# Kernel optimization log

Measured on AMD Instinct MI355X. Metric: run time of the kernel, lower is better.

The kernel has to match this reference:

```python
import jax, jax.numpy as jnp
import numpy as np
import math
from jax import lax

HID, H, K = 1024, 8, 4
D = HID // H
B, T = 2, 2048
CLAMP_MAX = 0.999995
LN_EPS = 1e-5

def _logit(x):
    x = min(max(x, 1e-06), 1 - 1e-06)
    return math.log(x / (1 - x))

def setup_inputs() -> dict:
    key = jax.random.key(0)
    ks = jax.random.split(key, 8)
    def xavier(k, fan_in, fan_out):
        s = math.sqrt(2.0 / (fan_in + fan_out))
        return jax.random.normal(k, (fan_in, fan_out), jnp.float32) * s
    x = jax.random.normal(ks[0], (B, T, HID), jnp.float32)
    mask = jnp.ones((B, T), jnp.float32)
    Wq = xavier(ks[1], HID, HID)
    Wk = xavier(ks[2], HID, HID)
    Wv = xavier(ks[3], HID, HID)
    Wb = xavier(ks[4], HID, H)
    bb = jnp.full((H,), _logit(0.99), jnp.float32)
    Wm = xavier(ks[5], HID, H * K)
    bm = jnp.zeros((H * K,), jnp.float32)
    Wo = xavier(ks[6], HID, HID)
    bo = jnp.zeros((HID,), jnp.float32)
    base = np.array([_logit(math.exp(-1.0 / t)) for t in [16.0, 64.0, 256.0, 1024.0]], np.float32)
    base_logit = jnp.asarray(np.tile(base[None, :], (H, 1)))  # (H, K)
    ln_g = jnp.ones((HID,), jnp.float32)
    ln_b = jnp.zeros((HID,), jnp.float32)
    return dict(x=x, mask=mask, Wq=Wq, Wk=Wk, Wv=Wv, Wb=Wb, bb=bb, Wm=Wm, bm=bm,
                Wo=Wo, bo=bo, base_logit=base_logit, ln_g=ln_g, ln_b=ln_b)

def _delta_scan(q, k, v, beta, mix, mask, base_logit):
    # q,k,v: (B,T,H,D); beta: (B,T,H); mix: (B,T,H,K); mask: (B,T)
    b, t = q.shape[0], q.shape[1]
    base_r = jax.nn.sigmoid(base_logit)  # (H,K)
    state0 = jnp.zeros((b, H, K, D, D), jnp.float32)

    def step(state, inp):
        q_t, k_t, v_t, b_t, mix_t, m_t = inp
        valid = (m_t > 0)[:, None, None, None, None]            # (B,1,1,1,1)
        r_eff = jnp.clip(b_t[:, :, None] * base_r[None], 0.0, CLAMP_MAX)  # (B,H,K)
        outer = jnp.einsum('bhd,bhe->bhde', k_t, v_t)[:, :, None]          # (B,H,1,D,D)
        new_state = jnp.where(valid, state * r_eff[..., None, None] + outer, state)
        o_scales = jnp.einsum('bhd,bhkde->bhke', q_t, new_state)           # (B,H,K,D)
        w = jax.nn.softmax(mix_t, axis=-1)                                  # (B,H,K)
        o_t = jnp.sum(w[..., None] * o_scales, axis=2)                      # (B,H,D)
        o_t = o_t * (m_t > 0)[:, None, None].astype(o_t.dtype)
        return new_state, o_t

    xs = (jnp.moveaxis(q, 1, 0), jnp.moveaxis(k, 1, 0), jnp.moveaxis(v, 1, 0),
          jnp.moveaxis(beta, 1, 0), jnp.moveaxis(mix, 1, 0), jnp.moveaxis(mask, 1, 0))
    _, outs = lax.scan(step, state0, xs)       # (T,B,H,D)
    return jnp.moveaxis(outs, 0, 1)            # (B,T,H,D)

def reference(x, mask, Wq, Wk, Wv, Wb, bb, Wm, bm, Wo, bo, base_logit, ln_g, ln_b):
    b, t, _ = x.shape
    def elu1(z):
        return jax.nn.elu(z) + 1.0
    q = elu1((x @ Wq).reshape(b, t, H, D))
    k = elu1((x @ Wk).reshape(b, t, H, D))
    v = (x @ Wv).reshape(b, t, H, D)
    beta = jax.nn.sigmoid(x @ Wb + bb)               # (B,T,H)
    mix = (x @ Wm + bm).reshape(b, t, H, K)          # (B,T,H,K)
    head_out = _delta_scan(q, k, v, beta, mix, mask, base_logit)  # (B,T,H,D)
    out = head_out.reshape(b, t, HID) @ Wo + bo
    y = x + out                                       # residual (dropout in eval mode)
    mu = jnp.mean(y, axis=-1, keepdims=True)
    var = jnp.mean((y - mu) ** 2, axis=-1, keepdims=True)
    return (y - mu) * lax.rsqrt(var + LN_EPS) * ln_g + ln_b
```

## Files before the change

### kernel.cpp

```cpp
#include <hip/hip_runtime.h>
#include <hip/hip_bf16.h>
#include <math.h>

#define TSEQ 2048
#define NHID 1024

typedef float f32x4 __attribute__((ext_vector_type(4)));
typedef __bf16 bf16x8 __attribute__((ext_vector_type(8)));

static __device__ __forceinline__ unsigned short f2bf(float f) {
  unsigned u = __float_as_uint(f);
  u += 0x7fffu + ((u >> 16) & 1u);
  return (unsigned short)(u >> 16);
}
static __device__ __forceinline__ float bf2f(unsigned short h) {
  return __uint_as_float(((unsigned)h) << 16);
}

#define GLDS16(g, l) __builtin_amdgcn_global_load_lds( \
    (const __attribute__((address_space(1))) unsigned int*)(g), \
    (__attribute__((address_space(3))) unsigned int*)(l), 16, 0, 0)

__global__ __launch_bounds__(256) void transpose_all_kernel(
    const float* __restrict__ Wq, const float* __restrict__ Wk,
    const float* __restrict__ Wv, const float* __restrict__ Wo,
    unsigned short* __restrict__ Wqkvt, unsigned short* __restrict__ Wto) {
  __shared__ float tile[32][33];
  const float* W;
  unsigned short* Wt;
  int m = blockIdx.z;
  if (m == 0)      { W = Wq; Wt = Wqkvt; }
  else if (m == 1) { W = Wk; Wt = Wqkvt + 1024 * 1024; }
  else if (m == 2) { W = Wv; Wt = Wqkvt + 2 * 1024 * 1024; }
  else             { W = Wo; Wt = Wto; }
  int bx = blockIdx.x * 32;
  int by = blockIdx.y * 32;
  int tx = threadIdx.x, ty = threadIdx.y;
#pragma unroll
  for (int i = 0; i < 32; i += 8)
    tile[ty + i][tx] = W[(size_t)(by + ty + i) * NHID + bx + tx];
  __syncthreads();
#pragma unroll
  for (int i = 0; i < 32; i += 8)
    Wt[(size_t)(bx + ty + i) * NHID + by + tx] = f2bf(tile[tx][ty + i]);
}

template <int MODE>
__global__ __launch_bounds__(256) void gemm_pipe_kernel(
    const unsigned short* __restrict__ A, const unsigned short* __restrict__ Bt,
    unsigned short* __restrict__ Oq, unsigned short* __restrict__ Ok,
    unsigned short* __restrict__ Ov, float* __restrict__ P0, float* __restrict__ P1) {
  __shared__ __align__(16) unsigned short As[3 * 4096];
  __shared__ __align__(16) unsigned short Bs[3 * 4096];
  const int tid = threadIdx.x;
  const int lane = tid & 63;
  const int wave = tid >> 6;
  const int wr = wave >> 1, wc = wave & 1;
  const int rowBase = blockIdx.y * 128;
  const int colBase = blockIdx.x * 128;
  const int NT = (MODE == 0) ? 32 : 16;
  const int kOff = (MODE == 0) ? 0 : blockIdx.z * 512;

  const int c0 = wave * 128 + lane;
  const int c1 = c0 + 64;
  const int r0 = c0 >> 2, kc0 = (c0 & 3) ^ ((r0 >> 1) & 3);
  const int r1 = c1 >> 2, kc1 = (c1 & 3) ^ ((r1 >> 1) & 3);
  const unsigned short* gA0 = A + (size_t)(rowBase + r0) * 1024 + kOff + kc0 * 8;
  const unsigned short* gA1 = A + (size_t)(rowBase + r1) * 1024 + kOff + kc1 * 8;
  const unsigned short* gB0 = Bt + (size_t)(colBase + r0) * 1024 + kOff + kc0 * 8;
  const unsigned short* gB1 = Bt + (size_t)(colBase + r1) * 1024 + kOff + kc1 * 8;
  const int wofs = wave * 1024;

  const int kq = lane >> 4;
  const int r16 = lane & 15;

  f32x4 acc[4][4] = {};

#define STAGE(buf, k0)                                       \
  do {                                                       \
    GLDS16(gA0 + (k0), &As[(buf) * 4096 + wofs]);            \
    GLDS16(gA1 + (k0), &As[(buf) * 4096 + wofs + 512]);      \
    GLDS16(gB0 + (k0), &Bs[(buf) * 4096 + wofs]);            \
    GLDS16(gB1 + (k0), &Bs[(buf) * 4096 + wofs + 512]);      \
  } while (0)

  STAGE(0, 0);
  STAGE(1, 32);
  int cur = 0, stg = 2;
  for (int t = 0; t < NT; ++t) {
    if (t < NT - 2) {
      STAGE(stg, (t + 2) * 32);
      asm volatile("s_waitcnt vmcnt(8)" ::: "memory");
    } else if (t == NT - 2) {
      asm volatile("s_waitcnt vmcnt(4)" ::: "memory");
    } else {
      asm volatile("s_waitcnt vmcnt(0)" ::: "memory");
    }
    __builtin_amdgcn_s_barrier();
    asm volatile("" ::: "memory");
    const unsigned short* Ac = &As[cur * 4096];
    const unsigned short* Bc = &Bs[cur * 4096];
    bf16x8 af[4], bfr[4];
#pragma unroll
    for (int m = 0; m < 4; ++m) {
      int row = wr * 64 + m * 16 + r16;
      af[m] = *(const bf16x8*)(Ac + row * 32 + (kq ^ ((row >> 1) & 3)) * 8);
      int colr = wc * 64 + m * 16 + r16;
      bfr[m] = *(const bf16x8*)(Bc + colr * 32 + (kq ^ ((colr >> 1) & 3)) * 8);
    }
#pragma unroll
    for (int m = 0; m < 4; ++m)
#pragma unroll
      for (int n = 0; n < 4; ++n)
        acc[m][n] = __builtin_amdgcn_mfma_f32_16x16x32_bf16(af[m], bfr[n], acc[m][n], 0, 0, 0);
    asm volatile("" ::: "memory");
    __builtin_amdgcn_s_barrier();
    asm volatile("" ::: "memory");
    cur = (cur == 2) ? 0 : cur + 1;
    stg = (stg == 2) ? 0 : stg + 1;
  }
#undef STAGE

  const int r4 = (lane >> 4) * 4;
  if (MODE == 1) {
    float* P = (blockIdx.z == 0) ? P0 : P1;
#pragma unroll
    for (int m = 0; m < 4; ++m)
#pragma unroll
      for (int n = 0; n < 4; ++n) {
        int col = colBase + wc * 64 + n * 16 + r16;
#pragma unroll
        for (int j = 0; j < 4; ++j) {
          int row = rowBase + wr * 64 + m * 16 + r4 + j;
          P[(size_t)row * 1024 + col] = acc[m][n][j];
        }
      }
  } else {
    unsigned short* outp;
    int cb;
    bool elu;
    if (colBase < 1024)      { outp = Oq; cb = colBase;        elu = true;  }
    else if (colBase < 2048) { outp = Ok; cb = colBase - 1024; elu = true;  }
    else                     { outp = Ov; cb = colBase - 2048; elu = false; }
#pragma unroll
    for (int m = 0; m < 4; ++m)
#pragma unroll
      for (int n = 0; n < 4; ++n) {
        int col = cb + wc * 64 + n * 16 + r16;
#pragma unroll
        for (int j = 0; j < 4; ++j) {
          int row = rowBase + wr * 64 + m * 16 + r4 + j;
          float v = acc[m][n][j];
          if (elu) v = (v > 0.f) ? (v + 1.f) : expf(v);
          outp[(size_t)row * 1024 + col] = f2bf(v);
        }
      }
  }
}

__global__ __launch_bounds__(256) void pack_wbm_kernel(const float* __restrict__ Wb,
    const float* __restrict__ Wm, float* __restrict__ Wt) {
  int id = blockIdx.x * 256 + threadIdx.x;
  if (id >= 40960) return;
  int o = id >> 10, i = id & 1023;
  Wt[id] = (o < 8) ? Wb[i * 8 + o] : Wm[i * 32 + (o - 8)];
}

__global__ __launch_bounds__(256) void rw8_kernel(const float* __restrict__ x,
    const float* __restrict__ Wt, const float* __restrict__ bb,
    const float* __restrict__ bm, const float* __restrict__ base_logit,
    float* __restrict__ R, float* __restrict__ Wsm,
    unsigned short* __restrict__ Xb) {
  __shared__ float xs[8][1024];
  __shared__ float outs[8][40];
  int row0 = blockIdx.x * 8;
  int tid = threadIdx.x;
#pragma unroll
  for (int r = 0; r < 8; ++r) {
    float4 xv = *(const float4*)(x + (size_t)(row0 + r) * 1024 + tid * 4);
    *(float4*)(&xs[r][tid * 4]) = xv;
    ushort4 xo;
    xo.x = f2bf(xv.x); xo.y = f2bf(xv.y); xo.z = f2bf(xv.z); xo.w = f2bf(xv.w);
    *(ushort4*)(Xb + (size_t)(row0 + r) * 1024 + tid * 4) = xo;
  }
  __syncthreads();
  int wave = tid >> 6, lane = tid & 63;
  for (int o = wave; o < 40; o += 4) {
    const float* wr = Wt + o * 1024;
    float w[16];
#pragma unroll
    for (int it = 0; it < 16; ++it) w[it] = wr[it * 64 + lane];
#pragma unroll
    for (int r = 0; r < 8; ++r) {
      float sum = 0.f;
#pragma unroll
      for (int it = 0; it < 16; ++it) sum += xs[r][it * 64 + lane] * w[it];
#pragma unroll
      for (int off = 32; off > 0; off >>= 1) sum += __shfl_down(sum, off);
      if (lane == 0) outs[r][o] = sum;
    }
  }
  __syncthreads();
  {
    int r = tid >> 5, j = tid & 31;
    int row = row0 + r;
    int h = j >> 2;
    float beta = 1.f / (1.f + expf(-(outs[r][h] + bb[h])));
    float br = 1.f / (1.f + expf(-base_logit[j]));
    float rr = fminf(fmaxf(beta * br, 0.f), 0.999995f);
    float mval = outs[r][8 + j] + bm[j];
    float mx = fmaxf(mval, __shfl_xor(mval, 1));
    mx = fmaxf(mx, __shfl_xor(mx, 2));
    float ex = expf(mval - mx);
    float ssum = ex + __shfl_xor(ex, 1);
    ssum += __shfl_xor(ssum, 2);
    R[(size_t)row * 32 + j] = rr;
    Wsm[(size_t)row * 32 + j] = ex / ssum;
  }
}

__global__ __launch_bounds__(256) void decay2_kernel(const float* __restrict__ R,
    const float* __restrict__ Wsm, const float* __restrict__ mask,
    float* __restrict__ WA, float* __restrict__ IA, float* __restrict__ DU,
    float* __restrict__ AC) {
  int wave = threadIdx.x >> 6, lane = threadIdx.x & 63;
  int id = blockIdx.x * 4 + wave;
  int c = id & 15, k = (id >> 4) & 3, bh = id >> 6;
  int b = bh >> 3, h = bh & 7;
  int row0 = b * TSEQ + c * 128 + 2 * lane;
  float m0 = mask[row0], m1 = mask[row0 + 1];
  size_t i0 = (size_t)row0 * 32 + h * 4 + k;
  float rr0 = (m0 > 0.f) ? R[i0] : 1.f;
  float rr1 = (m1 > 0.f) ? R[i0 + 32] : 1.f;
  float incl = rr0 * rr1;
#pragma unroll
  for (int off = 1; off < 64; off <<= 1) {
    float o = __shfl_up(incl, off);
    if (lane >= off) incl *= o;
  }
  float excl = __shfl_up(incl, 1);
  if (lane == 0) excl = 1.f;
  float a0 = fmaxf(excl * rr0, 1e-25f);
  float a1 = fmaxf(a0 * rr1, 1e-25f);
  float aC = __shfl(a1, 63);
  if (lane == 63) AC[(bh * 16 + c) * 4 + k] = a1;
  bool v0 = m0 > 0.f, v1 = m1 > 0.f;
  float w0 = Wsm[i0], w1 = Wsm[i0 + 32];
  int dub = ((bh * 16 + c) * 4 + k) * 128 + 2 * lane;
  WA[i0] = v0 ? w0 * a0 : 0.f;
  WA[i0 + 32] = v1 ? w1 * a1 : 0.f;
  IA[i0] = v0 ? 1.f / a0 : 0.f;
  IA[i0 + 32] = v1 ? 1.f / a1 : 0.f;
  DU[dub] = v0 ? aC / a0 : 0.f;
  DU[dub + 1] = v1 ? aC / a1 : 0.f;
}

__global__ __launch_bounds__(512) void chunkA_kernel(
    const unsigned short* __restrict__ Qb, const unsigned short* __restrict__ Kb,
    const unsigned short* __restrict__ Vb,
    const float* __restrict__ WA, const float* __restrict__ IA,
    const float* __restrict__ DU,
    float* __restrict__ Olocal, unsigned short* __restrict__ UT) {
  __shared__ __align__(16) char KTl[32768];
  __shared__ __align__(16) char VTl[32768];
  __shared__ __align__(16) char Pl[32768];
  __shared__ __align__(16) float WAl[128][4];
  __shared__ __align__(16) float IAl[128][4];
  __shared__ float DUl[4][128];

  int wg = blockIdx.x;
  int bh = wg >> 4, c = wg & 15;
  int b = bh >> 3, h = bh & 7;
  int t0 = c * 128;
  int tid = threadIdx.x;
  int lane = tid & 63, wave = tid >> 6;
  int wbase = wave * 16;
  int l15 = lane & 15, lq = lane >> 4;

  const size_t qkvbase = ((size_t)b * TSEQ + t0) * 1024 + h * 128;

  for (int it = 0; it < 4; ++it) {
    int ci = tid + it * 512;
    int t = ci >> 4, s = ci & 15;
    bf16x8 kv = *(const bf16x8*)(Kb + qkvbase + (size_t)t * 1024 + s * 8);
    bf16x8 vv = *(const bf16x8*)(Vb + qkvbase + (size_t)t * 1024 + s * 8);
#pragma unroll
    for (int e = 0; e < 8; ++e) {
      int d = s * 8 + e;
      int off = d * 256 + (((t >> 3) ^ (d & 7)) << 4) + (t & 7) * 2;
      *(unsigned short*)(KTl + off) = f2bf((float)kv[e]);
      *(unsigned short*)(VTl + off) = f2bf((float)vv[e]);
    }
  }
  {
    int t = tid >> 2, k = tid & 3;
    size_t idx = ((size_t)b * TSEQ + t0 + t) * 32 + h * 4 + k;
    WAl[t][k] = WA[idx];
    IAl[t][k] = IA[idx];
    int k2 = tid >> 7, j = tid & 127;
    DUl[k2][j] = DU[((bh * 16 + c) * 4 + k2) * 128 + j];
  }
  __syncthreads();

  bf16x8 qf[4];
#pragma unroll
  for (int ds = 0; ds < 4; ++ds)
    qf[ds] = *(const bf16x8*)(Qb + qkvbase + (size_t)(wbase + l15) * 1024 + ds * 32 + lq * 8);
  f32x4 accP[8];
#pragma unroll
  for (int jf = 0; jf < 8; ++jf) {
    f32x4 a = {};
#pragma unroll
    for (int ds = 0; ds < 4; ++ds) {
      bf16x8 kfrag = *(const bf16x8*)(Kb + qkvbase + (size_t)(jf * 16 + l15) * 1024 + ds * 32 + lq * 8);
      a = __builtin_amdgcn_mfma_f32_16x16x32_bf16(qf[ds], kfrag, a, 0, 0, 0);
    }
    accP[jf] = a;
  }

  float4 wa4[4];
#pragma unroll
  for (int jj = 0; jj < 4; ++jj)
    wa4[jj] = *(const float4*)&WAl[wbase + lq * 4 + jj][0];
#pragma unroll
  for (int jf = 0; jf < 8; ++jf) {
    float4 ia4 = *(const float4*)&IAl[jf * 16 + l15][0];
#pragma unroll
    for (int jj = 0; jj < 4; ++jj) {
      int tl = wbase + lq * 4 + jj;
      int jl = jf * 16 + l15;
      float m = 0.f;
      if (jl <= tl)
        m = wa4[jj].x * ia4.x + wa4[jj].y * ia4.y + wa4[jj].z * ia4.z + wa4[jj].w * ia4.w;
      float pv = accP[jf][jj] * m;
      int off = tl * 256 + (((jl >> 3) ^ (tl & 7)) << 4) + (jl & 7) * 2;
      *(unsigned short*)(Pl + off) = f2bf(pv);
    }
  }

  bf16x8 pf[4];
#pragma unroll
  for (int js = 0; js < 4; ++js) {
    int tl = wbase + l15;
    int slot = js * 4 + lq;
    pf[js] = *(const bf16x8*)(Pl + tl * 256 + ((slot ^ (tl & 7)) << 4));
  }
#pragma unroll
  for (int dvf = 0; dvf < 8; ++dvf) {
    f32x4 a = {};
    int dv = dvf * 16 + l15;
#pragma unroll
    for (int js = 0; js < 4; ++js) {
      int slot = js * 4 + lq;
      bf16x8 vfrag = *(const bf16x8*)(VTl + dv * 256 + ((slot ^ (dv & 7)) << 4));
      a = __builtin_amdgcn_mfma_f32_16x16x32_bf16(pf[js], vfrag, a, 0, 0, 0);
    }
#pragma unroll
    for (int jj = 0; jj < 4; ++jj) {
      int tl = wbase + lq * 4 + jj;
      Olocal[((size_t)b * TSEQ + t0 + tl) * 1024 + h * 128 + dv] = a[jj];
    }
  }

  if (c < 15) {
#pragma unroll 1
    for (int k = 0; k < 4; ++k) {
      f32x4 accU[8] = {};
#pragma unroll 1
      for (int js = 0; js < 4; ++js) {
        int dvr = wbase + l15;
        int slot = js * 4 + lq;
        bf16x8 af = *(const bf16x8*)(VTl + dvr * 256 + ((slot ^ (dvr & 7)) << 4));
        int j0 = js * 32 + lq * 8;
        bf16x8 afs;
#pragma unroll
        for (int e = 0; e < 8; ++e)
          afs[e] = (__bf16)((float)af[e] * DUl[k][j0 + e]);
#pragma unroll
        for (int dkf = 0; dkf < 8; ++dkf) {
          int dk = dkf * 16 + l15;
          bf16x8 kf = *(const bf16x8*)(KTl + dk * 256 + ((slot ^ (dk & 7)) << 4));
          accU[dkf] = __builtin_amdgcn_mfma_f32_16x16x32_bf16(afs, kf, accU[dkf], 0, 0, 0);
        }
      }
      size_t ub = (((size_t)bh * 16 + c) * 4 + k) * 16384;
#pragma unroll
      for (int dkf = 0; dkf < 8; ++dkf) {
        int dk = dkf * 16 + l15;
#pragma unroll
        for (int jj = 0; jj < 4; ++jj) {
          int dvr = wbase + lq * 4 + jj;
          UT[ub + (size_t)dvr * 128 + dk] = f2bf(accU[dkf][jj]);
        }
      }
    }
  }
}

__global__ __launch_bounds__(256) void chainB_kernel(const unsigned short* __restrict__ UT,
    const float* __restrict__ AC, unsigned short* __restrict__ S0T) {
  int id = blockIdx.x * 256 + threadIdx.x;
  int dk = id & 127;
  int dv = (id >> 7) & 127;
  int k = (id >> 14) & 3;
  int bh = id >> 16;
  size_t elem = (size_t)dv * 128 + dk;
  float S = 0.f;
#pragma unroll 1
  for (int c = 0; c < 15; ++c) {
    size_t ub = (((size_t)bh * 16 + c) * 4 + k) * 16384;
    float u = bf2f(UT[ub + elem]);
    float aC = AC[(bh * 16 + c) * 4 + k];
    S = aC * S + u;
    size_t sb = (((size_t)bh * 16 + (c + 1)) * 4 + k) * 16384;
    S0T[sb + elem] = f2bf(S);
  }
}

__global__ __launch_bounds__(512) void chunkC_kernel(const unsigned short* __restrict__ Qb,
    const unsigned short* __restrict__ S0T, const float* __restrict__ WA,
    const float* __restrict__ Olocal, unsigned short* __restrict__ Ob) {
  __shared__ __align__(16) char Sl[32768];
  int wg = blockIdx.x;
  int bh = wg >> 4, c = wg & 15;
  int b = bh >> 3, h = bh & 7;
  int t0 = c * 128;
  int tid = threadIdx.x, lane = tid & 63, wave = tid >> 6;
  int l15 = lane & 15, lq = lane >> 4, wbase = wave * 16;
  size_t qbase = ((size_t)b * TSEQ + t0) * 1024 + h * 128;

  f32x4 accO[8] = {};
  if (c > 0) {
    int tl = wbase + l15;
#pragma unroll 1
    for (int k = 0; k < 4; ++k) {
      __syncthreads();
      size_t sb = (((size_t)bh * 16 + c) * 4 + k) * 16384;
      for (int it = 0; it < 4; ++it) {
        int ci = tid + it * 512;
        int dv = ci >> 4, s = ci & 15;
        bf16x8 vv = *(const bf16x8*)(S0T + sb + (size_t)dv * 128 + s * 8);
        *(bf16x8*)(Sl + dv * 256 + ((s ^ (dv & 7)) << 4)) = vv;
      }
      __syncthreads();
      float sc = WA[((size_t)b * TSEQ + t0 + tl) * 32 + h * 4 + k];
#pragma unroll 1
      for (int ds = 0; ds < 4; ++ds) {
        bf16x8 qf = *(const bf16x8*)(Qb + qbase + (size_t)tl * 1024 + ds * 32 + lq * 8);
        bf16x8 qs;
#pragma unroll
        for (int e = 0; e < 8; ++e) qs[e] = (__bf16)((float)qf[e] * sc);
#pragma unroll
        for (int dvf = 0; dvf < 8; ++dvf) {
          int dv = dvf * 16 + l15;
          int slot = ds * 4 + lq;
          bf16x8 sf = *(const bf16x8*)(Sl + dv * 256 + ((slot ^ (dv & 7)) << 4));
          accO[dvf] = __builtin_amdgcn_mfma_f32_16x16x32_bf16(qs, sf, accO[dvf], 0, 0, 0);
        }
      }
    }
  }
#pragma unroll
  for (int dvf = 0; dvf < 8; ++dvf) {
    int dv = dvf * 16 + l15;
#pragma unroll
    for (int jj = 0; jj < 4; ++jj) {
      int tl = wbase + lq * 4 + jj;
      size_t off = ((size_t)b * TSEQ + t0 + tl) * 1024 + h * 128 + dv;
      Ob[off] = f2bf(accO[dvf][jj] + Olocal[off]);
    }
  }
}

__global__ __launch_bounds__(256) void ln_kernel(const float* __restrict__ P0,
    const float* __restrict__ P1, const float* __restrict__ bo,
    const float* __restrict__ xres,
    const float* __restrict__ g, const float* __restrict__ bta,
    float* __restrict__ out) {
  int row = blockIdx.x;
  int tid = threadIdx.x;
  int lane = tid & 63, wave = tid >> 6;
  __shared__ float red[8];
  size_t base = (size_t)row * 1024 + tid * 4;
  float4 a = *(const float4*)(P0 + base);
  float4 b2 = *(const float4*)(P1 + base);
  float4 xv = *(const float4*)(xres + base);
  float4 bv = *(const float4*)(bo + tid * 4);
  float4 v;
  v.x = a.x + b2.x + bv.x + xv.x;
  v.y = a.y + b2.y + bv.y + xv.y;
  v.z = a.z + b2.z + bv.z + xv.z;
  v.w = a.w + b2.w + bv.w + xv.w;
  float sum = v.x + v.y + v.z + v.w;
#pragma unroll
  for (int off = 32; off > 0; off >>= 1) sum += __shfl_down(sum, off);
  if (lane == 0) red[wave] = sum;
  __syncthreads();
  float mu = (red[0] + red[1] + red[2] + red[3]) * (1.f / 1024.f);
  float4 d;
  d.x = v.x - mu; d.y = v.y - mu; d.z = v.z - mu; d.w = v.w - mu;
  float sq = d.x * d.x + d.y * d.y + d.z * d.z + d.w * d.w;
#pragma unroll
  for (int off = 32; off > 0; off >>= 1) sq += __shfl_down(sq, off);
  __syncthreads();
  if (lane == 0) red[4 + wave] = sq;
  __syncthreads();
  float var = (red[4] + red[5] + red[6] + red[7]) * (1.f / 1024.f);
  float inv = rsqrtf(var + 1e-5f);
  float4 gg = *(const float4*)(g + tid * 4);
  float4 bb4 = *(const float4*)(bta + tid * 4);
  float4 o;
  o.x = d.x * inv * gg.x + bb4.x;
  o.y = d.y * inv * gg.y + bb4.y;
  o.z = d.z * inv * gg.z + bb4.z;
  o.w = d.w * inv * gg.w + bb4.w;
  *(float4*)(out + (size_t)row * 1024 + tid * 4) = o;
}

extern "C" void kernel_launch(void* const* d_in, const int* in_sizes, int n_in,
                              void* d_out, int out_size, void* d_ws, size_t ws_size,
                              hipStream_t stream) {
  const float* x    = (const float*)d_in[0];
  const float* mask = (const float*)d_in[1];
  const float* Wq   = (const float*)d_in[2];
  const float* Wk   = (const float*)d_in[3];
  const float* Wv   = (const float*)d_in[4];
  const float* Wb   = (const float*)d_in[5];
  const float* bb   = (const float*)d_in[6];
  const float* Wm   = (const float*)d_in[7];
  const float* bm   = (const float*)d_in[8];
  const float* Wo   = (const float*)d_in[9];
  const float* bo   = (const float*)d_in[10];
  const float* base_logit = (const float*)d_in[11];
  const float* ln_g = (const float*)d_in[12];
  const float* ln_b = (const float*)d_in[13];

  char* ws = (char*)d_ws;
  const size_t MB = 1024u * 1024u;
  unsigned short* Xb    = (unsigned short*)(ws + 0);
  unsigned short* Wqkvt = (unsigned short*)(ws + 8 * MB);
  unsigned short* Wto   = (unsigned short*)(ws + 14 * MB);
  float* Rf  = (float*)(ws + 16 * MB);
  float* Wsf = (float*)(ws + 16 * MB + 512 * 1024);
  float* WAf = (float*)(ws + 17 * MB);
  float* IAf = (float*)(ws + 17 * MB + 512 * 1024);
  float* DUf = (float*)(ws + 18 * MB);
  float* ACf = (float*)(ws + 18 * MB + 512 * 1024);
  float* Wtf = (float*)(ws + 18 * MB + 768 * 1024);
  unsigned short* Qb = (unsigned short*)(ws + 19 * MB);
  unsigned short* Kb = (unsigned short*)(ws + 27 * MB);
  unsigned short* Vb = (unsigned short*)(ws + 35 * MB);
  float* Olocal = (float*)(ws + 43 * MB);
  unsigned short* Ob = (unsigned short*)(ws + 59 * MB);
  unsigned short* UTb = (unsigned short*)(ws + 67 * MB);
  unsigned short* S0T = (unsigned short*)(ws + 99 * MB);
  float* Pp0 = Olocal;
  float* Pp1 = (float*)(ws + 67 * MB);
  if (ws_size < 131 * MB) return;

  dim3 tb(32, 8), tg(32, 32, 4);
  transpose_all_kernel<<<tg, tb, 0, stream>>>(Wq, Wk, Wv, Wo, Wqkvt, Wto);
  pack_wbm_kernel<<<160, 256, 0, stream>>>(Wb, Wm, Wtf);

  rw8_kernel<<<512, 256, 0, stream>>>(x, Wtf, bb, bm, base_logit, Rf, Wsf, Xb);
  decay2_kernel<<<256, 256, 0, stream>>>(Rf, Wsf, mask, WAf, IAf, DUf, ACf);

  dim3 gqkv(24, 32);
  gemm_pipe_kernel<0><<<gqkv, 256, 0, stream>>>(Xb, Wqkvt, Qb, Kb, Vb, nullptr, nullptr);

  chunkA_kernel<<<256, 512, 0, stream>>>(Qb, Kb, Vb, WAf, IAf, DUf, Olocal, UTb);
  chainB_kernel<<<4096, 256, 0, stream>>>(UTb, ACf, S0T);
  chunkC_kernel<<<256, 512, 0, stream>>>(Qb, S0T, WAf, Olocal, Ob);

  dim3 gwo(8, 32, 2);
  gemm_pipe_kernel<1><<<gwo, 256, 0, stream>>>(Ob, Wto, nullptr, nullptr, nullptr, Pp0, Pp1);

  ln_kernel<<<4096, 256, 0, stream>>>(Pp0, Pp1, bo, x, ln_g, ln_b, (float*)d_out);
}
```

Baseline: 175.3 us.

## Replace QKV projection GEMM with 256x256-tile, 8-wave, quarter-pipelined kernel

The fused QKV projection GEMM moves from 128x128 tiles with 4 waves to 256x256 tiles with 8 waves and a K-step of 64. Operand loads are split into half-tiles and interleaved with four MFMA quarter phases, raising wave priority around the MFMAs. A block-index swizzle groups neighbouring tiles for L2 reuse, and a wider XOR LDS swizzle is used. The grid shrinks to 192 blocks, fewer than the CU count, which risks underusing the device in exchange for higher arithmetic intensity per block.

```diff
diff --git a/kernel.cpp b/kernel.cpp
--- a/kernel.cpp
+++ b/kernel.cpp
@@ -45,11 +45,147 @@
     Wt[(size_t)(bx + ty + i) * NHID + by + tx] = f2bf(tile[tx][ty + i]);
 }
 
-template <int MODE>
-__global__ __launch_bounds__(256) void gemm_pipe_kernel(
+__global__ __launch_bounds__(512) void gemm8p_kernel(
     const unsigned short* __restrict__ A, const unsigned short* __restrict__ Bt,
     unsigned short* __restrict__ Oq, unsigned short* __restrict__ Ok,
-    unsigned short* __restrict__ Ov, float* __restrict__ P0, float* __restrict__ P1) {
+    unsigned short* __restrict__ Ov) {
+  __shared__ __align__(16) unsigned short As[2][16384];
+  __shared__ __align__(16) unsigned short Bs[2][16384];
+  const int tid = threadIdx.x;
+  const int lane = tid & 63;
+  const int wave = tid >> 6;
+  const int wr = wave >> 2;
+  const int wc = wave & 3;
+  const int kq = lane >> 4;
+  const int r16 = lane & 15;
+  const int lswz = r16 & 7;
+
+  const int nbxy = gridDim.x * gridDim.y;
+  const int lin = blockIdx.y * gridDim.x + blockIdx.x;
+  const int bswz = (lin & 7) * (nbxy >> 3) + (lin >> 3);
+  const int rowBase = (bswz / gridDim.x) * 256;
+  const int colBase = (bswz % gridDim.x) * 256;
+
+  const int c0 = wave * 128 + lane, c1 = c0 + 64;
+  const int lr0 = c0 >> 3, kc0 = (c0 & 7) ^ (lr0 & 7);
+  const int lr1 = c1 >> 3, kc1 = (c1 & 7) ^ (lr1 & 7);
+  const unsigned short* gA_0 = A + (size_t)(rowBase + lr0) * 1024 + kc0 * 8;
+  const unsigned short* gA_1 = A + (size_t)(rowBase + lr1) * 1024 + kc1 * 8;
+  const unsigned short* gB_0 = Bt + (size_t)(colBase + lr0) * 1024 + kc0 * 8;
+  const unsigned short* gB_1 = Bt + (size_t)(colBase + lr1) * 1024 + kc1 * 8;
+  const int wldso = wave * 1024;
+
+#define STAGE_A(ts, h) do { \
+    GLDS16(gA_0 + (size_t)(h) * 131072 + (ts) * 64, &As[(ts) & 1][(h) * 8192 + wldso]); \
+    GLDS16(gA_1 + (size_t)(h) * 131072 + (ts) * 64, &As[(ts) & 1][(h) * 8192 + wldso + 512]); \
+  } while (0)
+#define STAGE_B(ts, h) do { \
+    GLDS16(gB_0 + (size_t)(h) * 131072 + (ts) * 64, &Bs[(ts) & 1][(h) * 8192 + wldso]); \
+    GLDS16(gB_1 + (size_t)(h) * 131072 + (ts) * 64, &Bs[(ts) & 1][(h) * 8192 + wldso + 512]); \
+  } while (0)
+#define READ_T(base, r, kk) (*(const bf16x8*)((const char*)(base) + (r) * 128 + (((((kk) << 2) | kq) ^ lswz) << 4)))
+
+  f32x4 acc[8][4] = {};
+
+  STAGE_A(0, 0); STAGE_B(0, 0); STAGE_B(0, 1); STAGE_A(0, 1);
+  STAGE_A(1, 0); STAGE_B(1, 0);
+  asm volatile("s_waitcnt vmcnt(8)" ::: "memory");
+  __builtin_amdgcn_s_barrier();
+  asm volatile("" ::: "memory");
+
+#pragma unroll 1
+  for (int kt = 0; kt < 16; ++kt) {
+    const unsigned short* Ab = &As[kt & 1][0];
+    const unsigned short* Bb = &Bs[kt & 1][0];
+    bf16x8 af[4][2], bf[2][2][2];
+#pragma unroll
+    for (int q = 0; q < 4; ++q) {
+      const int mh = q >> 1, nh = q & 1;
+      if (q == 0) {
+#pragma unroll
+        for (int n = 0; n < 2; ++n)
+#pragma unroll
+          for (int kk = 0; kk < 2; ++kk)
+            bf[0][n][kk] = READ_T(Bb, wc * 32 + n * 16 + r16, kk);
+#pragma unroll
+        for (int m = 0; m < 4; ++m)
+#pragma unroll
+          for (int kk = 0; kk < 2; ++kk)
+            af[m][kk] = READ_T(Ab, wr * 64 + m * 16 + r16, kk);
+      } else if (q == 1) {
+#pragma unroll
+        for (int n = 0; n < 2; ++n)
+#pragma unroll
+          for (int kk = 0; kk < 2; ++kk)
+            bf[1][n][kk] = READ_T(Bb, 128 + wc * 32 + n * 16 + r16, kk);
+      } else if (q == 2) {
+#pragma unroll
+        for (int m = 0; m < 4; ++m)
+#pragma unroll
+          for (int kk = 0; kk < 2; ++kk)
+            af[m][kk] = READ_T(Ab, 128 + wr * 64 + m * 16 + r16, kk);
+      }
+      if (q == 0) { if (kt + 1 < 16) STAGE_B(kt + 1, 1); }
+      else if (q == 1) { if (kt + 1 < 16) STAGE_A(kt + 1, 1); }
+      else if (q == 2) { if (kt + 2 < 16) STAGE_A(kt + 2, 0); }
+      else             { if (kt + 2 < 16) STAGE_B(kt + 2, 0); }
+      if (kt < 14) {
+        asm volatile("s_waitcnt vmcnt(8)" ::: "memory");
+      } else if (kt == 14) {
+        if (q <= 1) asm volatile("s_waitcnt vmcnt(8)" ::: "memory");
+        else if (q == 2) asm volatile("s_waitcnt vmcnt(6)" ::: "memory");
+        else asm volatile("s_waitcnt vmcnt(4)" ::: "memory");
+      } else {
+        if (q == 0) asm volatile("s_waitcnt vmcnt(2)" ::: "memory");
+        else asm volatile("s_waitcnt vmcnt(0)" ::: "memory");
+      }
+      __builtin_amdgcn_s_barrier();
+      asm volatile("" ::: "memory");
+      __builtin_amdgcn_s_setprio(1);
+#pragma unroll
+      for (int m = 0; m < 4; ++m)
+#pragma unroll
+        for (int n = 0; n < 2; ++n)
+#pragma unroll
+          for (int kk = 0; kk < 2; ++kk)
+            acc[mh * 4 + m][nh * 2 + n] = __builtin_amdgcn_mfma_f32_16x16x32_bf16(
+                af[m][kk], bf[nh][n][kk], acc[mh * 4 + m][nh * 2 + n], 0, 0, 0);
+      __builtin_amdgcn_s_setprio(0);
+      asm volatile("" ::: "memory");
+      __builtin_amdgcn_s_barrier();
+      asm volatile("" ::: "memory");
+    }
+  }
+#undef STAGE_A
+#undef STAGE_B
+#undef READ_T
+
+  const int r4 = (lane >> 4) * 4;
+  unsigned short* outp;
+  int cb;
+  bool elu;
+  if (colBase < 1024)      { outp = Oq; cb = colBase;        elu = true;  }
+  else if (colBase < 2048) { outp = Ok; cb = colBase - 1024; elu = true;  }
+  else                     { outp = Ov; cb = colBase - 2048; elu = false; }
+#pragma unroll
+  for (int m = 0; m < 8; ++m) {
+    int rbase = rowBase + (m >> 2) * 128 + wr * 64 + (m & 3) * 16 + r4;
+#pragma unroll
+    for (int n = 0; n < 4; ++n) {
+      int col = cb + (n >> 1) * 128 + wc * 32 + (n & 1) * 16 + r16;
+#pragma unroll
+      for (int j = 0; j < 4; ++j) {
+        float v = acc[m][n][j];
+        if (elu) v = (v > 0.f) ? (v + 1.f) : expf(v);
+        outp[(size_t)(rbase + j) * 1024 + col] = f2bf(v);
+      }
+    }
+  }
+}
+
+__global__ __launch_bounds__(256) void gemm_wo_kernel(
+    const unsigned short* __restrict__ A, const unsigned short* __restrict__ Bt,
+    float* __restrict__ P0, float* __restrict__ P1) {
   __shared__ __align__(16) unsigned short As[3 * 4096];
   __shared__ __align__(16) unsigned short Bs[3 * 4096];
   const int tid = threadIdx.x;
@@ -58,8 +194,7 @@
   const int wr = wave >> 1, wc = wave & 1;
   const int rowBase = blockIdx.y * 128;
   const int colBase = blockIdx.x * 128;
-  const int NT = (MODE == 0) ? 32 : 16;
-  const int kOff = (MODE == 0) ? 0 : blockIdx.z * 512;
+  const int kOff = blockIdx.z * 512;
 
   const int c0 = wave * 128 + lane;
   const int c1 = c0 + 64;
@@ -87,11 +222,11 @@
   STAGE(0, 0);
   STAGE(1, 32);
   int cur = 0, stg = 2;
-  for (int t = 0; t < NT; ++t) {
-    if (t < NT - 2) {
+  for (int t = 0; t < 16; ++t) {
+    if (t < 14) {
       STAGE(stg, (t + 2) * 32);
       asm volatile("s_waitcnt vmcnt(8)" ::: "memory");
-    } else if (t == NT - 2) {
+    } else if (t == 14) {
       asm volatile("s_waitcnt vmcnt(4)" ::: "memory");
     } else {
       asm volatile("s_waitcnt vmcnt(0)" ::: "memory");
@@ -122,40 +257,18 @@
 #undef STAGE
 
   const int r4 = (lane >> 4) * 4;
-  if (MODE == 1) {
-    float* P = (blockIdx.z == 0) ? P0 : P1;
-#pragma unroll
-    for (int m = 0; m < 4; ++m)
-#pragma unroll
-      for (int n = 0; n < 4; ++n) {
-        int col = colBase + wc * 64 + n * 16 + r16;
-#pragma unroll
-        for (int j = 0; j < 4; ++j) {
-          int row = rowBase + wr * 64 + m * 16 + r4 + j;
-          P[(size_t)row * 1024 + col] = acc[m][n][j];
-        }
-      }
-  } else {
-    unsigned short* outp;
-    int cb;
-    bool elu;
-    if (colBase < 1024)      { outp = Oq; cb = colBase;        elu = true;  }
-    else if (colBase < 2048) { outp = Ok; cb = colBase - 1024; elu = true;  }
-    else                     { outp = Ov; cb = colBase - 2048; elu = false; }
-#pragma unroll
-    for (int m = 0; m < 4; ++m)
-#pragma unroll
-      for (int n = 0; n < 4; ++n) {
-        int col = cb + wc * 64 + n * 16 + r16;
-#pragma unroll
-        for (int j = 0; j < 4; ++j) {
-          int row = rowBase + wr * 64 + m * 16 + r4 + j;
-          float v = acc[m][n][j];
-          if (elu) v = (v > 0.f) ? (v + 1.f) : expf(v);
-          outp[(size_t)row * 1024 + col] = f2bf(v);
-        }
-      }
-  }
+  float* P = (blockIdx.z == 0) ? P0 : P1;
+#pragma unroll
+  for (int m = 0; m < 4; ++m)
+#pragma unroll
+    for (int n = 0; n < 4; ++n) {
+      int col = colBase + wc * 64 + n * 16 + r16;
+#pragma unroll
+      for (int j = 0; j < 4; ++j) {
+        int row = rowBase + wr * 64 + m * 16 + r4 + j;
+        P[(size_t)row * 1024 + col] = acc[m][n][j];
+      }
+    }
 }
 
 __global__ __launch_bounds__(256) void pack_wbm_kernel(const float* __restrict__ Wb,
@@ -565,15 +678,15 @@
   rw8_kernel<<<512, 256, 0, stream>>>(x, Wtf, bb, bm, base_logit, Rf, Wsf, Xb);
   decay2_kernel<<<256, 256, 0, stream>>>(Rf, Wsf, mask, WAf, IAf, DUf, ACf);
 
-  dim3 gqkv(24, 32);
-  gemm_pipe_kernel<0><<<gqkv, 256, 0, stream>>>(Xb, Wqkvt, Qb, Kb, Vb, nullptr, nullptr);
+  dim3 gqkv(12, 16);
+  gemm8p_kernel<<<gqkv, 512, 0, stream>>>(Xb, Wqkvt, Qb, Kb, Vb);
 
   chunkA_kernel<<<256, 512, 0, stream>>>(Qb, Kb, Vb, WAf, IAf, DUf, Olocal, UTb);
   chainB_kernel<<<4096, 256, 0, stream>>>(UTb, ACf, S0T);
   chunkC_kernel<<<256, 512, 0, stream>>>(Qb, S0T, WAf, Olocal, Ob);
 
   dim3 gwo(8, 32, 2);
-  gemm_pipe_kernel<1><<<gwo, 256, 0, stream>>>(Ob, Wto, nullptr, nullptr, nullptr, Pp0, Pp1);
+  gemm_wo_kernel<<<gwo, 256, 0, stream>>>(Ob, Wto, Pp0, Pp1);
 
   ln_kernel<<<4096, 256, 0, stream>>>(Pp0, Pp1, bo, x, ln_g, ln_b, (float*)d_out);
 }
```

After: 183.4 us. 1.05x slower.
